# Kernel tuning notes

Hardware: AMD Instinct MI355X
Metric: run time of the kernel (lower is better)

The kernel has to match this reference:

```python
import jax, jax.numpy as jnp
import numpy as np

EPS = 1e-5          # InstanceNorm eps (torch default)
KERNEL = 25         # moving_avg_kernel_size
TAU = 1.0           # gumbel softmax temperature
REGIME_NUM = 8


def _inorm(x):
    # InstanceNorm1d without affine on (N, C, L): normalize over last dim (biased var)
    m = x.mean(-1, keepdims=True)
    v = ((x - m) ** 2).mean(-1, keepdims=True)
    return (x - m) * jax.lax.rsqrt(v + EPS)


def _lbr(x, W, b):
    # Linear -> InstanceNorm (over last dim) -> exact GELU
    return jax.nn.gelu(_inorm(x @ W + b), approximate=False)


def _moving_avg(x, k):
    # x: (B, L, C); edge-replicate pad (k-1)//2 on both sides, sliding mean via cumsum
    p = (k - 1) // 2
    xp = jnp.concatenate([jnp.repeat(x[:, :1], p, axis=1), x,
                          jnp.repeat(x[:, -1:], p, axis=1)], axis=1)
    cs = jnp.concatenate([jnp.zeros_like(xp[:, :1]), jnp.cumsum(xp, axis=1)], axis=1)
    return (cs[:, k:] - cs[:, :-k]) / k  # (B, L, C)


def _encode(x, Ws, bs, Wt, bt):
    # inputs - inputs[:, 0:1]; series decomposition; seasonal+trend branches
    x = x - x[:, :1]
    mm = _moving_avg(x, KERNEL)
    return _lbr(x - mm, Ws, bs) + _lbr(mm, Wt, bt)  # (B, L, H)


def reference(inputs_longterm, inputs_shortterm,
              Ws, bs, Wt, bt,
              Wh1, bh1, Wl1, bl1, Wh2, bh2, Wl2, bl2, Wh3, bh3, Wl3, bl3,
              Wr, br, proto):
    e_lt = _encode(inputs_longterm, Ws, bs, Wt, bt)   # (B, L_lt, H)
    e_st = _encode(inputs_shortterm, Ws, bs, Wt, bt)  # (B, L_st, H)

    # RegimeEncoder: alternate hidden-dim and lookback-dim LinearBatchRelu layers
    o = _lbr(e_lt, Wh1, bh1)
    o = jnp.swapaxes(_lbr(jnp.swapaxes(o, 1, 2), Wl1, bl1), 1, 2)
    o = _lbr(o, Wh2, bh2)
    o = jnp.swapaxes(_lbr(jnp.swapaxes(o, 1, 2), Wl2, bl2), 1, 2)
    o = _lbr(o, Wh3, bh3)
    o = jnp.swapaxes(_lbr(jnp.swapaxes(o, 1, 2), Wl3, bl3), 1, 2)  # (B, L_lt//8, H)
    logits = o.reshape(o.shape[0], -1) @ Wr + br  # (B, R)

    # gumbel_softmax(hard=True) with straight-through estimator
    g = jax.random.gumbel(jax.random.key(42), logits.shape, logits.dtype)
    y_soft = jax.nn.softmax((logits + g) / TAU, axis=-1)
    y_hard = jax.nn.one_hot(jnp.argmax(y_soft, axis=-1), REGIME_NUM, dtype=logits.dtype)
    w = y_hard - jax.lax.stop_gradient(y_soft) + y_soft  # (B, R)

    # weighted sum over regime prototypes, then combine with encoded shortterm
    sel = jnp.einsum('br,rnhmo->bnhmo', w, proto)          # (B, L_st, H, M, 3)
    out = jnp.einsum('bnh,bnhmo->bmo', e_st, sel)          # (B, M, 3)
    B = out.shape[0]
    return jax.nn.softmax(out.reshape(B, -1), axis=-1).reshape(out.shape)


def setup_inputs() -> dict:
    key = jax.random.key(0)
    ks = jax.random.split(key, 24)
    B, L_lt, L_st, C, H, R, M = 32, 512, 128, 9, 128, 8, 64
    s = 0.02
    d = {
        'inputs_longterm':  jax.random.normal(ks[0], (B, L_lt, C), jnp.float32),
        'inputs_shortterm': jax.random.normal(ks[1], (B, L_st, C), jnp.float32),
        'Ws': jax.random.normal(ks[2], (C, H), jnp.float32) * s,
        'bs': jnp.zeros((H,), jnp.float32),
        'Wt': jax.random.normal(ks[3], (C, H), jnp.float32) * s,
        'bt': jnp.zeros((H,), jnp.float32),
        'Wh1': jax.random.normal(ks[4], (H, H), jnp.float32) * s,
        'bh1': jnp.zeros((H,), jnp.float32),
        'Wl1': jax.random.normal(ks[5], (L_lt, L_lt // 2), jnp.float32) * s,
        'bl1': jnp.zeros((L_lt // 2,), jnp.float32),
        'Wh2': jax.random.normal(ks[6], (H, H), jnp.float32) * s,
        'bh2': jnp.zeros((H,), jnp.float32),
        'Wl2': jax.random.normal(ks[7], (L_lt // 2, L_lt // 4), jnp.float32) * s,
        'bl2': jnp.zeros((L_lt // 4,), jnp.float32),
        'Wh3': jax.random.normal(ks[8], (H, H), jnp.float32) * s,
        'bh3': jnp.zeros((H,), jnp.float32),
        'Wl3': jax.random.normal(ks[9], (L_lt // 4, L_lt // 8), jnp.float32) * s,
        'bl3': jnp.zeros((L_lt // 8,), jnp.float32),
        'Wr': jax.random.normal(ks[10], (H * L_lt // 8, R), jnp.float32) * s,
        'br': jnp.zeros((R,), jnp.float32),
        'proto': jax.random.normal(ks[11], (R, L_st, H, M, 3), jnp.float32),
    }
    return d
```

## Files before the change

kernel.cpp:

```cpp
#include <hip/hip_runtime.h>
#include <math.h>

#define EPS 1e-5f

__device__ __forceinline__ float gelu_exact(float x) {
    return 0.5f * x * (1.0f + erff(x * 0.7071067811865476f));
}

__device__ float block_sum(float v, float* red) {
    int lane = threadIdx.x & 63, wid = threadIdx.x >> 6;
#pragma unroll
    for (int off = 32; off > 0; off >>= 1) v += __shfl_down(v, off, 64);
    if (lane == 0) red[wid] = v;
    __syncthreads();
    int nw = ((int)blockDim.x + 63) >> 6;
    float s = red[0];
    for (int w = 1; w < nw; w++) s += red[w];
    __syncthreads();
    return s;
}

__device__ float block_max(float v, float* red) {
    int lane = threadIdx.x & 63, wid = threadIdx.x >> 6;
#pragma unroll
    for (int off = 32; off > 0; off >>= 1) v = fmaxf(v, __shfl_down(v, off, 64));
    if (lane == 0) red[wid] = v;
    __syncthreads();
    int nw = ((int)blockDim.x + 63) >> 6;
    float s = red[0];
    for (int w = 1; w < nw; w++) s = fmaxf(s, red[w]);
    __syncthreads();
    return s;
}

__device__ void threefry2x32(unsigned k0, unsigned k1, unsigned x0, unsigned x1,
                             unsigned& o0, unsigned& o1) {
    unsigned ks[3] = {k0, k1, k0 ^ k1 ^ 0x1BD11BDAu};
    const unsigned rot[2][4] = {{13u, 15u, 26u, 6u}, {17u, 29u, 16u, 24u}};
    x0 += ks[0]; x1 += ks[1];
#pragma unroll
    for (int i = 0; i < 5; i++) {
#pragma unroll
        for (int j = 0; j < 4; j++) {
            unsigned r = rot[i & 1][j];
            x0 += x1;
            x1 = (x1 << r) | (x1 >> (32 - r));
            x1 ^= x0;
        }
        x0 += ks[(i + 1) % 3];
        x1 += ks[(i + 2) % 3] + (unsigned)(i + 1);
    }
    o0 = x0; o1 = x1;
}

__device__ float gumbel_at(int j) {
    unsigned o0, o1;
    threefry2x32(0u, 42u, 0u, (unsigned)j, o0, o1);
    unsigned bits = o0 ^ o1;
    float f = __uint_as_float((bits >> 9) | 0x3F800000u) - 1.0f;
    float u = fmaxf(f + 1.17549435e-38f, 1.17549435e-38f);
    return -logf(-logf(u));
}

__global__ __launch_bounds__(256) void encode_kernel(
    const float* __restrict__ x_lt, const float* __restrict__ x_st,
    const float* __restrict__ Ws, const float* __restrict__ bs,
    const float* __restrict__ Wt, const float* __restrict__ bt,
    float* __restrict__ e_lt, float* __restrict__ e_st) {
    const int b = blockIdx.y;
    const int w = threadIdx.x >> 6, ln = threadIdx.x & 63;
    const float* x; float* e; int L, l;
    if (blockIdx.x < 128) { x = x_lt; e = e_lt; L = 512; l = blockIdx.x * 4 + w; }
    else { x = x_st; e = e_st; L = 128; l = (blockIdx.x - 128) * 4 + w; }
    __shared__ float xw_all[4][228];
    __shared__ float sm_all[4][20];
    float* xw = xw_all[w];
    float* sm = sm_all[w];
    const float* xb = x + (size_t)b * L * 9;
#pragma unroll
    for (int q = 0; q < 4; q++) {
        int f = ln + 64 * q;
        if (f < 225) {
            int row = f / 9, c = f - row * 9;
            int rr = l - 12 + row;
            rr = rr < 0 ? 0 : (rr >= L ? L - 1 : rr);
            xw[f] = xb[(size_t)rr * 9 + c];
        }
    }
    __syncthreads();
    if (ln < 9) {
        float s = 0.f;
#pragma unroll
        for (int j = 0; j < 25; j++) s += xw[j * 9 + ln];
        float x0 = xb[ln];
        float mm = (s - 25.f * x0) * (1.0f / 25.0f);
        sm[ln] = (xw[108 + ln] - x0) - mm;
        sm[ln + 10] = mm;
    }
    __syncthreads();
    float ysA = bs[ln], ysB = bs[ln + 64];
    float ytA = bt[ln], ytB = bt[ln + 64];
#pragma unroll
    for (int c = 0; c < 9; c++) {
        float sv = sm[c], mv = sm[c + 10];
        ysA += sv * Ws[c * 128 + ln];
        ysB += sv * Ws[c * 128 + ln + 64];
        ytA += mv * Wt[c * 128 + ln];
        ytB += mv * Wt[c * 128 + ln + 64];
    }
    float sa = ysA + ysB, sb2 = ytA + ytB;
#pragma unroll
    for (int off = 32; off > 0; off >>= 1) {
        sa += __shfl_xor(sa, off, 64);
        sb2 += __shfl_xor(sb2, off, 64);
    }
    float ms = sa * (1.0f / 128.0f), mt = sb2 * (1.0f / 128.0f);
    float dA = ysA - ms, dB = ysB - ms;
    float tA = ytA - mt, tB = ytB - mt;
    float qa = dA * dA + dB * dB, qb = tA * tA + tB * tB;
#pragma unroll
    for (int off = 32; off > 0; off >>= 1) {
        qa += __shfl_xor(qa, off, 64);
        qb += __shfl_xor(qb, off, 64);
    }
    float inva = rsqrtf(qa * (1.0f / 128.0f) + EPS);
    float invb = rsqrtf(qb * (1.0f / 128.0f) + EPS);
    float* eo = e + ((size_t)b * L + l) * 128;
    eo[ln] = gelu_exact(dA * inva) + gelu_exact(tA * invb);
    eo[ln + 64] = gelu_exact(dB * inva) + gelu_exact(tB * invb);
}

template <int K, int N, int WR, bool TRANS>
__global__ __launch_bounds__(256) void lbr_wave(
    const float* __restrict__ A, int S, int ABOFF,
    const float* __restrict__ W, const float* __restrict__ bias,
    float* __restrict__ out, int OROWS, int OBOFF) {
    constexpr int CG = N / 4;
    constexpr int SG = 64 / CG;
    constexpr int RW = SG * WR;
    constexpr int MT = 4 * RW;
    constexpr int LOG2MT = (MT == 8) ? 3 : ((MT == 16) ? 4 : 5);
    constexpr int STAGE = 4 * RW * K;
    constexpr int TILE = TRANS ? MT * (N + 4) : 0;
    constexpr int LSZ = STAGE > TILE ? STAGE : TILE;
    __shared__ __align__(16) float lds[LSZ];
    const int t = threadIdx.x;
    const int w = t >> 6, ln = t & 63;
    const int sg = ln / CG;
    const int n0 = (ln % CG) * 4;
    const int b = blockIdx.y;
    const int r0b = blockIdx.x * MT;
    const int r0w = r0b + w * RW;
    float* As = lds + w * RW * K;
    const float* Ab = A + (size_t)b * ABOFF;
    for (int idx = ln; idx < RW * (K / 4); idx += 64) {
        int rr = idx / (K / 4), kk = idx % (K / 4);
        float4 v = *(const float4*)(Ab + (size_t)(r0w + rr) * S + kk * 4);
        *(float4*)(As + rr * K + kk * 4) = v;
    }
    float4 acc[WR];
    {
        float4 bv = *(const float4*)(bias + n0);
#pragma unroll
        for (int j = 0; j < WR; j++) acc[j] = bv;
    }
    const float* ap = As + (sg * WR) * K;
    const float* wp = W + n0;
#pragma unroll 2
    for (int k = 0; k < K; k += 4) {
        float4 w0 = *(const float4*)(wp);
        float4 w1 = *(const float4*)(wp + N);
        float4 w2 = *(const float4*)(wp + 2 * N);
        float4 w3 = *(const float4*)(wp + 3 * N);
        wp += 4 * N;
#pragma unroll
        for (int j = 0; j < WR; j++) {
            float4 a4 = *(const float4*)(ap + j * K + k);
            acc[j].x += a4.x * w0.x; acc[j].y += a4.x * w0.y;
            acc[j].z += a4.x * w0.z; acc[j].w += a4.x * w0.w;
            acc[j].x += a4.y * w1.x; acc[j].y += a4.y * w1.y;
            acc[j].z += a4.y * w1.z; acc[j].w += a4.y * w1.w;
            acc[j].x += a4.z * w2.x; acc[j].y += a4.z * w2.y;
            acc[j].z += a4.z * w2.z; acc[j].w += a4.z * w2.w;
            acc[j].x += a4.w * w3.x; acc[j].y += a4.w * w3.y;
            acc[j].z += a4.w * w3.z; acc[j].w += a4.w * w3.w;
        }
    }
    float4 res[WR];
#pragma unroll
    for (int j = 0; j < WR; j++) {
        float s = acc[j].x + acc[j].y + acc[j].z + acc[j].w;
#pragma unroll
        for (int off = CG / 2; off > 0; off >>= 1) s += __shfl_xor(s, off, 64);
        float m = s * (1.0f / (float)N);
        float dx = acc[j].x - m, dy = acc[j].y - m, dz = acc[j].z - m, dw = acc[j].w - m;
        float q = dx * dx + dy * dy + dz * dz + dw * dw;
#pragma unroll
        for (int off = CG / 2; off > 0; off >>= 1) q += __shfl_xor(q, off, 64);
        float inv = rsqrtf(q * (1.0f / (float)N) + EPS);
        res[j].x = gelu_exact(dx * inv);
        res[j].y = gelu_exact(dy * inv);
        res[j].z = gelu_exact(dz * inv);
        res[j].w = gelu_exact(dw * inv);
    }
    if constexpr (TRANS) {
        __syncthreads();
#pragma unroll
        for (int j = 0; j < WR; j++) {
            int rl = w * RW + sg * WR + j;
            *(float4*)(lds + rl * (N + 4) + n0) = res[j];
        }
        __syncthreads();
        float* ob = out + (size_t)b * OBOFF + r0b;
        for (int e = t; e < MT * N; e += 256) {
            int r = e & (MT - 1), n = e >> LOG2MT;
            ob[(size_t)n * OROWS + r] = lds[r * (N + 4) + n];
        }
    } else {
        float* ob = out + (size_t)b * OBOFF;
#pragma unroll
        for (int j = 0; j < WR; j++) {
            int row = r0w + sg * WR + j;
            *(float4*)(ob + (size_t)row * N + n0) = res[j];
        }
    }
}

__global__ __launch_bounds__(256) void logits_select(
    const float* __restrict__ O6, const float* __restrict__ Wr,
    const float* __restrict__ br, float* __restrict__ sel_w, int* __restrict__ sel_r) {
    int b = blockIdx.x, t = threadIdx.x;
    __shared__ float sO6[128 * 68];
    __shared__ float red[4][8];
    const float4* ob4 = (const float4*)(O6 + (size_t)b * 8192);
    for (int i4 = t; i4 < 2048; i4 += 256) {
        float4 v = ob4[i4];
        int p = i4 * 4;
        int h = p >> 6, l4 = p & 63;
        *(float4*)(&sO6[h * 68 + l4]) = v;
    }
    __syncthreads();
    float acc[8] = {0, 0, 0, 0, 0, 0, 0, 0};
#pragma unroll 4
    for (int q = 0; q < 32; q++) {
        int i = q * 256 + t;
        int l4 = i >> 7, h = i & 127;
        float v = sO6[h * 68 + l4];
        const float4* wr = (const float4*)(Wr + (size_t)i * 8);
        float4 w0 = wr[0], w1 = wr[1];
        acc[0] += v * w0.x; acc[1] += v * w0.y; acc[2] += v * w0.z; acc[3] += v * w0.w;
        acc[4] += v * w1.x; acc[5] += v * w1.y; acc[6] += v * w1.z; acc[7] += v * w1.w;
    }
#pragma unroll
    for (int j = 0; j < 8; j++)
#pragma unroll
        for (int off = 32; off > 0; off >>= 1) acc[j] += __shfl_xor(acc[j], off, 64);
    int lane = t & 63, wid = t >> 6;
    if (lane == 0)
        for (int j = 0; j < 8; j++) red[wid][j] = acc[j];
    __syncthreads();
    if (t == 0) {
        float z[8];
        for (int j = 0; j < 8; j++) {
            float lg = br[j] + red[0][j] + red[1][j] + red[2][j] + red[3][j];
            z[j] = lg + gumbel_at(b * 8 + j);
        }
        int am = 0;
        float zm = z[0];
        for (int j = 1; j < 8; j++)
            if (z[j] > zm) { zm = z[j]; am = j; }
        float ssum = 0.f;
        for (int j = 0; j < 8; j++) ssum += expf(z[j] - zm);
        float s = 1.0f / ssum;
        sel_w[b] = (1.0f - s) + s;
        sel_r[b] = am;
    }
}

__global__ __launch_bounds__(192) void einsum_nsplit(
    const float* __restrict__ e_st, const float* __restrict__ proto,
    const int* __restrict__ sel_r, float* __restrict__ part) {
    const int n0 = blockIdx.x * 2, r = blockIdx.y, t = threadIdx.x;
    __shared__ int loc[32];
    __shared__ int s_gs;
    if (t == 0) {
        int g = 0;
        for (int bb = 0; bb < 32; bb++)
            if (sel_r[bb] == r) loc[g++] = bb;
        s_gs = g;
    }
    __syncthreads();
    const int gs = s_gs;
    if (gs == 0) return;
    __shared__ __align__(16) float es[2][8][128];
    const float* pb0 = proto + ((size_t)r * 128 + n0) * (128 * 192) + t;
    const float* pb1 = pb0 + 128 * 192;
    for (int s0 = 0; s0 < gs; s0 += 8) {
        int np = gs - s0 < 8 ? gs - s0 : 8;
        __syncthreads();
        for (int i4 = t; i4 < 512; i4 += 192) {
            int nn = i4 >> 8, rem = i4 & 255;
            int sb = rem >> 5, h4 = rem & 31;
            float4 v = make_float4(0.f, 0.f, 0.f, 0.f);
            if (sb < np) {
                int bb = loc[s0 + sb];
                v = ((const float4*)(e_st + ((size_t)bb * 128 + n0 + nn) * 128))[h4];
            }
            *(float4*)(&es[nn][sb][h4 * 4]) = v;
        }
        __syncthreads();
        float a0[8] = {0, 0, 0, 0, 0, 0, 0, 0};
        float a1[8] = {0, 0, 0, 0, 0, 0, 0, 0};
#pragma unroll 2
        for (int h = 0; h < 128; h += 4) {
            float p00 = pb0[(h + 0) * 192], p01 = pb0[(h + 1) * 192];
            float p02 = pb0[(h + 2) * 192], p03 = pb0[(h + 3) * 192];
            float p10 = pb1[(h + 0) * 192], p11 = pb1[(h + 1) * 192];
            float p12 = pb1[(h + 2) * 192], p13 = pb1[(h + 3) * 192];
#pragma unroll
            for (int sb = 0; sb < 8; sb++) {
                float4 e0 = *(const float4*)(&es[0][sb][h]);
                float4 e1 = *(const float4*)(&es[1][sb][h]);
                a0[sb] += e0.x * p00; a0[sb] += e0.y * p01;
                a0[sb] += e0.z * p02; a0[sb] += e0.w * p03;
                a1[sb] += e1.x * p10; a1[sb] += e1.y * p11;
                a1[sb] += e1.z * p12; a1[sb] += e1.w * p13;
            }
        }
#pragma unroll
        for (int sb = 0; sb < 8; sb++) {
            if (sb < np) {
                int bb = loc[s0 + sb];
                part[((size_t)bb * 128 + n0) * 192 + t] = a0[sb];
                part[((size_t)bb * 128 + n0 + 1) * 192 + t] = a1[sb];
            }
        }
    }
}

__global__ void finalize_kernel(const float* __restrict__ part, const float* __restrict__ sel_w,
                                float* __restrict__ out) {
    int b = blockIdx.x, t = threadIdx.x;
    __shared__ float red[4];
    float v = 0.f;
#pragma unroll 8
    for (int c = 0; c < 128; c++) v += part[((size_t)b * 128 + c) * 192 + t];
    v *= sel_w[b];
    float mx = block_max(v, red);
    float e = expf(v - mx);
    float s = block_sum(e, red);
    out[(size_t)b * 192 + t] = e / s;
}

extern "C" void kernel_launch(void* const* d_in, const int* in_sizes, int n_in,
                              void* d_out, int out_size, void* d_ws, size_t ws_size,
                              hipStream_t stream) {
    const float* in_lt = (const float*)d_in[0];
    const float* in_st = (const float*)d_in[1];
    const float* Ws  = (const float*)d_in[2];  const float* bs  = (const float*)d_in[3];
    const float* Wt  = (const float*)d_in[4];  const float* bt  = (const float*)d_in[5];
    const float* Wh1 = (const float*)d_in[6];  const float* bh1 = (const float*)d_in[7];
    const float* Wl1 = (const float*)d_in[8];  const float* bl1 = (const float*)d_in[9];
    const float* Wh2 = (const float*)d_in[10]; const float* bh2 = (const float*)d_in[11];
    const float* Wl2 = (const float*)d_in[12]; const float* bl2 = (const float*)d_in[13];
    const float* Wh3 = (const float*)d_in[14]; const float* bh3 = (const float*)d_in[15];
    const float* Wl3 = (const float*)d_in[16]; const float* bl3 = (const float*)d_in[17];
    const float* Wr  = (const float*)d_in[18]; const float* br  = (const float*)d_in[19];
    const float* proto = (const float*)d_in[20];
    float* out = (float*)d_out;

    float* ws = (float*)d_ws;
    size_t off = 0;
    float* e_lt = ws + off; off += (size_t)32 * 512 * 128;
    float* e_st = ws + off; off += (size_t)32 * 128 * 128;
    float* O1T = ws + off; off += (size_t)128 * 16384;
    float* O2T = ws + off; off += (size_t)256 * 4096;
    float* O3T = ws + off; off += (size_t)128 * 8192;
    float* O4T = ws + off; off += (size_t)128 * 4096;
    float* O5T = ws + off; off += (size_t)128 * 4096;
    float* O6 = ws + off; off += (size_t)32 * 128 * 64;
    float* part = ws + off; off += (size_t)32 * 128 * 192;
    float* sel_w = ws + off; off += 32;
    int* sel_r = (int*)(ws + off); off += 32;

    encode_kernel<<<dim3(160, 32), 256, 0, stream>>>(in_lt, in_st, Ws, bs, Wt, bt, e_lt, e_st);
    lbr_wave<128, 128, 4, true><<<dim3(512, 1), 256, 0, stream>>>(
        e_lt, 128, 0, Wh1, bh1, O1T, 16384, 0);
    lbr_wave<512, 256, 4, true><<<dim3(8, 32), 256, 0, stream>>>(
        O1T, 16384, 512, Wl1, bl1, O2T, 4096, 128);
    lbr_wave<128, 128, 4, true><<<dim3(8, 32), 256, 0, stream>>>(
        O2T, 4096, 128, Wh2, bh2, O3T, 8192, 256);
    lbr_wave<256, 128, 2, true><<<dim3(8, 32), 256, 0, stream>>>(
        O3T, 8192, 256, Wl2, bl2, O4T, 4096, 128);
    lbr_wave<128, 128, 2, true><<<dim3(8, 32), 256, 0, stream>>>(
        O4T, 4096, 128, Wh3, bh3, O5T, 4096, 128);
    lbr_wave<128, 64, 1, false><<<dim3(8, 32), 256, 0, stream>>>(
        O5T, 4096, 128, Wl3, bl3, O6, 0, 8192);
    logits_select<<<32, 256, 0, stream>>>(O6, Wr, br, sel_w, sel_r);
    einsum_nsplit<<<dim3(64, 8), 192, 0, stream>>>(e_st, proto, sel_r, part);
    finalize_kernel<<<32, 192, 0, stream>>>(part, sel_w, out);
}
```

Measured before the change: 377.2 us.

## Split einsum over hidden halves and double grid for middle LBR layers

The prototype einsum kernel now gives each block one n and half of the H dimension, so the grid grows from 64x8 to 128x8x2. Partial sums go to two separate buffers that the finalize kernel adds together. The intermediate lbr_wave launches also halve their per-block row count and double the grid. The aim is more blocks in flight to hide memory latency on the large proto read, at the cost of a larger partial buffer and extra reads in finalize.

```diff
diff --git a/kernel.cpp b/kernel.cpp
--- a/kernel.cpp
+++ b/kernel.cpp
@@ -280,7 +280,7 @@
 __global__ __launch_bounds__(192) void einsum_nsplit(
     const float* __restrict__ e_st, const float* __restrict__ proto,
     const int* __restrict__ sel_r, float* __restrict__ part) {
-    const int n0 = blockIdx.x * 2, r = blockIdx.y, t = threadIdx.x;
+    const int n = blockIdx.x, r = blockIdx.y, hz = blockIdx.z, t = threadIdx.x;
     __shared__ int loc[32];
     __shared__ int s_gs;
     if (t == 0) {
@@ -292,47 +292,39 @@
     __syncthreads();
     const int gs = s_gs;
     if (gs == 0) return;
-    __shared__ __align__(16) float es[2][8][128];
-    const float* pb0 = proto + ((size_t)r * 128 + n0) * (128 * 192) + t;
-    const float* pb1 = pb0 + 128 * 192;
+    __shared__ __align__(16) float es[8][64];
+    const float* pb = proto + (((size_t)r * 128 + n) * 128 + hz * 64) * 192 + t;
+    float* po = part + (size_t)hz * (32 * 128 * 192);
     for (int s0 = 0; s0 < gs; s0 += 8) {
         int np = gs - s0 < 8 ? gs - s0 : 8;
         __syncthreads();
-        for (int i4 = t; i4 < 512; i4 += 192) {
-            int nn = i4 >> 8, rem = i4 & 255;
-            int sb = rem >> 5, h4 = rem & 31;
-            float4 v = make_float4(0.f, 0.f, 0.f, 0.f);
-            if (sb < np) {
-                int bb = loc[s0 + sb];
-                v = ((const float4*)(e_st + ((size_t)bb * 128 + n0 + nn) * 128))[h4];
-            }
-            *(float4*)(&es[nn][sb][h4 * 4]) = v;
+        for (int i = t; i < 512; i += 192) {
+            int sb = i >> 6, h = i & 63;
+            float v = 0.f;
+            if (sb < np)
+                v = e_st[((size_t)loc[s0 + sb] * 128 + n) * 128 + hz * 64 + h];
+            es[sb][h] = v;
         }
         __syncthreads();
-        float a0[8] = {0, 0, 0, 0, 0, 0, 0, 0};
-        float a1[8] = {0, 0, 0, 0, 0, 0, 0, 0};
-#pragma unroll 2
-        for (int h = 0; h < 128; h += 4) {
-            float p00 = pb0[(h + 0) * 192], p01 = pb0[(h + 1) * 192];
-            float p02 = pb0[(h + 2) * 192], p03 = pb0[(h + 3) * 192];
-            float p10 = pb1[(h + 0) * 192], p11 = pb1[(h + 1) * 192];
-            float p12 = pb1[(h + 2) * 192], p13 = pb1[(h + 3) * 192];
+        float a[8] = {0, 0, 0, 0, 0, 0, 0, 0};
+#pragma unroll
+        for (int h = 0; h < 64; h += 8) {
+            float p[8];
+#pragma unroll
+            for (int u = 0; u < 8; u++) p[u] = pb[(size_t)(h + u) * 192];
 #pragma unroll
             for (int sb = 0; sb < 8; sb++) {
-                float4 e0 = *(const float4*)(&es[0][sb][h]);
-                float4 e1 = *(const float4*)(&es[1][sb][h]);
-                a0[sb] += e0.x * p00; a0[sb] += e0.y * p01;
-                a0[sb] += e0.z * p02; a0[sb] += e0.w * p03;
-                a1[sb] += e1.x * p10; a1[sb] += e1.y * p11;
-                a1[sb] += e1.z * p12; a1[sb] += e1.w * p13;
+                float4 e0 = *(const float4*)(&es[sb][h]);
+                float4 e1 = *(const float4*)(&es[sb][h + 4]);
+                a[sb] += e0.x * p[0] + e0.y * p[1] + e0.z * p[2] + e0.w * p[3]
+                       + e1.x * p[4] + e1.y * p[5] + e1.z * p[6] + e1.w * p[7];
             }
         }
 #pragma unroll
         for (int sb = 0; sb < 8; sb++) {
             if (sb < np) {
                 int bb = loc[s0 + sb];
-                part[((size_t)bb * 128 + n0) * 192 + t] = a0[sb];
-                part[((size_t)bb * 128 + n0 + 1) * 192 + t] = a1[sb];
+                po[((size_t)bb * 128 + n) * 192 + t] = a[sb];
             }
         }
     }
@@ -342,9 +334,14 @@
                                 float* __restrict__ out) {
     int b = blockIdx.x, t = threadIdx.x;
     __shared__ float red[4];
+    const float* p0 = part + (size_t)b * 128 * 192 + t;
+    const float* p1 = p0 + (size_t)32 * 128 * 192;
     float v = 0.f;
 #pragma unroll 8
-    for (int c = 0; c < 128; c++) v += part[((size_t)b * 128 + c) * 192 + t];
+    for (int c = 0; c < 128; c++) {
+        v += p0[(size_t)c * 192];
+        v += p1[(size_t)c * 192];
+    }
     v *= sel_w[b];
     float mx = block_max(v, red);
     float e = expf(v - mx);
@@ -379,24 +376,24 @@
     float* O4T = ws + off; off += (size_t)128 * 4096;
     float* O5T = ws + off; off += (size_t)128 * 4096;
     float* O6 = ws + off; off += (size_t)32 * 128 * 64;
-    float* part = ws + off; off += (size_t)32 * 128 * 192;
+    float* part = ws + off; off += (size_t)2 * 32 * 128 * 192;
     float* sel_w = ws + off; off += 32;
     int* sel_r = (int*)(ws + off); off += 32;
 
     encode_kernel<<<dim3(160, 32), 256, 0, stream>>>(in_lt, in_st, Ws, bs, Wt, bt, e_lt, e_st);
     lbr_wave<128, 128, 4, true><<<dim3(512, 1), 256, 0, stream>>>(
         e_lt, 128, 0, Wh1, bh1, O1T, 16384, 0);
-    lbr_wave<512, 256, 4, true><<<dim3(8, 32), 256, 0, stream>>>(
+    lbr_wave<512, 256, 2, true><<<dim3(16, 32), 256, 0, stream>>>(
         O1T, 16384, 512, Wl1, bl1, O2T, 4096, 128);
-    lbr_wave<128, 128, 4, true><<<dim3(8, 32), 256, 0, stream>>>(
+    lbr_wave<128, 128, 2, true><<<dim3(16, 32), 256, 0, stream>>>(
         O2T, 4096, 128, Wh2, bh2, O3T, 8192, 256);
-    lbr_wave<256, 128, 2, true><<<dim3(8, 32), 256, 0, stream>>>(
+    lbr_wave<256, 128, 1, true><<<dim3(16, 32), 256, 0, stream>>>(
         O3T, 8192, 256, Wl2, bl2, O4T, 4096, 128);
-    lbr_wave<128, 128, 2, true><<<dim3(8, 32), 256, 0, stream>>>(
+    lbr_wave<128, 128, 1, true><<<dim3(16, 32), 256, 0, stream>>>(
         O4T, 4096, 128, Wh3, bh3, O5T, 4096, 128);
     lbr_wave<128, 64, 1, false><<<dim3(8, 32), 256, 0, stream>>>(
         O5T, 4096, 128, Wl3, bl3, O6, 0, 8192);
     logits_select<<<32, 256, 0, stream>>>(O6, Wr, br, sel_w, sel_r);
-    einsum_nsplit<<<dim3(64, 8), 192, 0, stream>>>(e_st, proto, sel_r, part);
+    einsum_nsplit<<<dim3(128, 8, 2), 192, 0, stream>>>(e_st, proto, sel_r, part);
     finalize_kernel<<<32, 192, 0, stream>>>(part, sel_w, out);
 }
```

After: 371.7 us. About the same (-1.5%).
